# Performance work log

Measured on AMD Instinct MI355X. Metric: run time of the kernel, lower is better.

The kernel has to match this reference:

```python
import jax, jax.numpy as jnp
import numpy as np

N_HEADS = 16


def setup_inputs() -> dict:
    key = jax.random.key(0)
    bs, width, length = 2, 3072, 2048  # width = 3 * n_heads * ch, ch = 64
    qkv = jax.random.normal(key, (bs, width, length), dtype=jnp.float32)
    return {"qkv": qkv}


def reference(qkv):
    bs, width, length = qkv.shape
    ch = width // (3 * N_HEADS)
    # per-head layout within width is [q(ch), k(ch), v(ch)]
    qkv_h = qkv.reshape(bs * N_HEADS, 3 * ch, length)
    q, k, v = jnp.split(qkv_h, 3, axis=1)  # each [bs*H, ch, L]
    scale = 1.0 / jnp.sqrt(jnp.sqrt(jnp.asarray(ch, dtype=qkv.dtype)))
    # scores: [bs*H, L_q, L_k]
    weight = jnp.einsum('bct,bcs->bts', q * scale, k * scale)
    weight = jax.nn.softmax(weight.astype(jnp.float32), axis=-1).astype(qkv.dtype)
    a = jnp.einsum('bts,bcs->bct', weight, v)  # [bs*H, ch, L]
    return a.reshape(bs, -1, length)
```

## Files before the change

### kernel.cpp

```cpp
#include <hip/hip_runtime.h>
#include <hip/hip_bf16.h>
#include <stdint.h>

typedef float f32x4 __attribute__((ext_vector_type(4)));
typedef float f32x16 __attribute__((ext_vector_type(16)));
typedef __bf16 bf16x8 __attribute__((ext_vector_type(8)));
typedef uint32_t u32;
typedef u32 u32x4 __attribute__((ext_vector_type(4)));

#define SCALE 0.35355339059327378f
#define SCALE2 0.42466090014400953f
#define LOG2E 1.4426950408889634f

#if __has_builtin(__builtin_amdgcn_exp2f)
__device__ __forceinline__ float exp2fast(float x) { return __builtin_amdgcn_exp2f(x); }
#else
__device__ __forceinline__ float exp2fast(float x) { return exp2f(x); }
#endif

__device__ __forceinline__ u32 packbf2(float a, float b) {
  u32 ua = __builtin_bit_cast(u32, a);
  u32 ub = __builtin_bit_cast(u32, b);
  ua = (ua + 0x7fffu + ((ua >> 16) & 1u)) >> 16;
  ub = (ub + 0x7fffu + ((ub >> 16) & 1u)) >> 16;
  return ua | (ub << 16);
}
__device__ __forceinline__ unsigned short tobf(float a) {
  u32 ua = __builtin_bit_cast(u32, a);
  return (unsigned short)((ua + 0x7fffu + ((ua >> 16) & 1u)) >> 16);
}
__device__ __forceinline__ u32 pk2(float a, float b) {
  unsigned short lo = __builtin_bit_cast(unsigned short, (__bf16)a);
  unsigned short hi = __builtin_bit_cast(unsigned short, (__bf16)b);
  return (u32)lo | ((u32)hi << 16);
}
__device__ __forceinline__ int swz(int row, int col) {
  return row * 64 + (col ^ ((row & 7) << 3));
}
__device__ __forceinline__ void gload16(const void* g, void* l) {
  __builtin_amdgcn_global_load_lds((const __attribute__((address_space(1))) void*)g,
                                   (__attribute__((address_space(3))) void*)l, 16, 0, 0);
}
__device__ __forceinline__ f32x16 zero16() {
  f32x16 z;
#pragma unroll
  for (int i = 0; i < 16; ++i) z[i] = 0.f;
  return z;
}

__global__ __launch_bounds__(256) void prep_kernel(const float* __restrict__ qkv,
                                                   unsigned short* __restrict__ ws) {
  __shared__ unsigned short tq[64 * 64];
  __shared__ unsigned short tk[64 * 64];
  const int tid = threadIdx.x;
  const int bid = blockIdx.x;
  const int bh = bid >> 5;
  const int tile = bid & 31;
  const int b = bh >> 4, h = bh & 15;
  const float* hq = qkv + ((size_t)b * 3072 + (size_t)h * 192) * 2048;
  const int s0 = tile * 64;

  {
    const int c = tid >> 2;
    const int jj = (tid & 3) * 16;
    const float* qp = hq + (size_t)c * 2048 + s0 + jj;
    const float* kp = qp + 64 * 2048;
    const float* vp = qp + 128 * 2048;
    unsigned short* vout = ws + (size_t)64 * 131072 + (size_t)bh * 131072 +
                           (size_t)c * 2048 + s0 + jj;
    u32 vbuf[8];
#pragma unroll
    for (int u = 0; u < 4; ++u) {
      f32x4 fq = *(const f32x4*)(qp + u * 4);
      f32x4 fk = *(const f32x4*)(kp + u * 4);
      f32x4 fv = *(const f32x4*)(vp + u * 4);
#pragma unroll
      for (int e = 0; e < 4; ++e) {
        int s = jj + u * 4 + e;
        int sw = swz(s, c);
        tq[sw] = tobf(fq[e] * SCALE2);
        tk[sw] = tobf(fk[e] * SCALE2);
      }
      vbuf[2 * u]     = packbf2(fv[0], fv[1]);
      vbuf[2 * u + 1] = packbf2(fv[2], fv[3]);
    }
    *(u32x4*)(vout)     = *(u32x4*)&vbuf[0];
    *(u32x4*)(vout + 8) = *(u32x4*)&vbuf[4];
  }
  __syncthreads();
  {
    const int s = tid >> 2;
    const int c0 = (tid & 3) * 16;
    const int ch0 = (((c0 >> 3) ^ (s & 7)) << 3);
    const int ch1 = ((((c0 >> 3) + 1) ^ (s & 7)) << 3);
    size_t ob = (size_t)bh * 131072 + (size_t)(s0 + s) * 64 + c0;
    unsigned short* qout = ws + ob;
    unsigned short* kout = ws + (size_t)32 * 131072 + ob;
    *(u32x4*)qout       = *(u32x4*)&tq[s * 64 + ch0];
    *(u32x4*)(qout + 8) = *(u32x4*)&tq[s * 64 + ch1];
    *(u32x4*)kout       = *(u32x4*)&tk[s * 64 + ch0];
    *(u32x4*)(kout + 8) = *(u32x4*)&tk[s * 64 + ch1];
  }
}

__global__ __launch_bounds__(512, 4) void attn15_kernel(const unsigned short* __restrict__ ws,
                                                        float* __restrict__ out) {
  __shared__ __align__(16) char smem[66560];

  const int tid  = threadIdx.x;
  const int lane = tid & 63;
  const int wv   = tid >> 6;
  const int w4   = wv & 3;
  const int grp  = wv >> 2;
  const int l31  = lane & 31;
  const int hi   = lane >> 5;
  const int xr   = l31 & 7;
  const int xr2  = (l31 >> 3) & 3;

  const int bid = blockIdx.x;
  const int bh  = (bid & 7) * 4 + ((bid >> 3) >> 4);
  const int qb  = (bid >> 3) & 15;
  const int b = bh >> 4, h = bh & 15;

  const unsigned short* Qs = ws + (size_t)bh * 131072;
  const unsigned short* Ks = ws + (size_t)32 * 131072 + (size_t)bh * 131072;
  const unsigned short* Vs = ws + (size_t)64 * 131072 + (size_t)bh * 131072;

  bf16x8 qB[4];
#pragma unroll
  for (int kc = 0; kc < 4; ++kc)
    qB[kc] = *(const bf16x8*)(Qs + (size_t)(qb * 128 + w4 * 32 + l31) * 64 + kc * 16 + hi * 8);

  const int srow = lane >> 3;
  const int xa   = (2 * w4) & 3;
  const int sch0 = (lane & 7) ^ srow ^ xa;
  const int sch1 = sch0 ^ 1;
  const char* kgA = (const char*)Ks + (size_t)(w4 * 16 + srow) * 128      + sch0 * 16;
  const char* kgB = (const char*)Ks + (size_t)(w4 * 16 + 8 + srow) * 128  + sch1 * 16;
  const char* vgA = (const char*)Vs + (size_t)(w4 * 16 + srow) * 4096     + sch0 * 16;
  const char* vgB = (const char*)Vs + (size_t)(w4 * 16 + 8 + srow) * 4096 + sch1 * 16;
  char* kbase = smem + grp * 16384;
  char* vbase = smem + 32768 + grp * 16384;
  char* kd = kbase + w4 * 2048;
  char* vd = vbase + w4 * 2048;

  f32x16 oacc0 = zero16(), oacc1 = zero16();
  float lrun = 0.f;

  {
    gload16(kgA + (size_t)grp * 8192, kd);
    gload16(kgB + (size_t)grp * 8192, kd + 1024);
    gload16(vgA + (size_t)grp * 128,  vd);
    gload16(vgB + (size_t)grp * 128,  vd + 1024);
  }

#pragma unroll 1
  for (int it = 0; it < 16; ++it) {
    const int cur = it & 1;
    __syncthreads();
    if (it < 15) {
      const int stn = 2 * (it + 1) + grp;
      char* kdn = kd + (cur ^ 1) * 8192;
      char* vdn = vd + (cur ^ 1) * 8192;
      gload16(kgA + (size_t)stn * 8192, kdn);
      gload16(kgB + (size_t)stn * 8192, kdn + 1024);
      gload16(vgA + (size_t)stn * 128,  vdn);
      gload16(vgB + (size_t)stn * 128,  vdn + 1024);
    }

    const unsigned short* kt = (const unsigned short*)(kbase + cur * 8192);
    f32x16 a0 = zero16(), a1 = zero16();
    __builtin_amdgcn_s_setprio(1);
#pragma unroll
    for (int kc = 0; kc < 4; ++kc) {
      int chs = (((kc * 2 + hi) ^ xr ^ xr2)) << 3;
      bf16x8 kA0 = *(const bf16x8*)(kt + l31 * 64 + chs);
      bf16x8 kA1 = *(const bf16x8*)(kt + (32 + l31) * 64 + chs);
      a0 = __builtin_amdgcn_mfma_f32_32x32x16_bf16(kA0, qB[kc], a0, 0, 0, 0);
      a1 = __builtin_amdgcn_mfma_f32_32x32x16_bf16(kA1, qB[kc], a1, 0, 0, 0);
    }
    __builtin_amdgcn_s_setprio(0);

#pragma unroll
    for (int i = 0; i < 16; ++i) a0[i] = exp2fast(a0[i]);
#pragma unroll
    for (int i = 0; i < 16; ++i) a1[i] = exp2fast(a1[i]);
    {
      f32x16 s01 = a0 + a1;
      f32x4 s4;
#pragma unroll
      for (int i = 0; i < 4; ++i)
        s4[i] = (s01[i] + s01[i + 4]) + (s01[i + 8] + s01[i + 12]);
      lrun += (s4[0] + s4[1]) + (s4[2] + s4[3]);
    }

    bf16x8 pB[4];
#pragma unroll
    for (int sc = 0; sc < 4; ++sc) {
      const f32x16& src = (sc < 2) ? a0 : a1;
      const int rb = (sc & 1) * 8;
      u32 c01 = pk2(src[rb + 0], src[rb + 1]);
      u32 c23 = pk2(src[rb + 2], src[rb + 3]);
      u32 c45 = pk2(src[rb + 4], src[rb + 5]);
      u32 c67 = pk2(src[rb + 6], src[rb + 7]);
      asm volatile("v_permlane32_swap_b32 %0, %1" : "+v"(c01), "+v"(c45));
      asm volatile("v_permlane32_swap_b32 %0, %1" : "+v"(c23), "+v"(c67));
      u32x4 w = {c01, c23, c45, c67};
      pB[sc] = __builtin_bit_cast(bf16x8, w);
    }

    const unsigned short* vt = (const unsigned short*)(vbase + cur * 8192);
    __builtin_amdgcn_s_setprio(1);
#pragma unroll
    for (int sc = 0; sc < 4; ++sc) {
      int chs = (((sc * 2 + hi) ^ xr ^ xr2)) << 3;
      bf16x8 vA0 = *(const bf16x8*)(vt + l31 * 64 + chs);
      bf16x8 vA1 = *(const bf16x8*)(vt + (32 + l31) * 64 + chs);
      oacc0 = __builtin_amdgcn_mfma_f32_32x32x16_bf16(vA0, pB[sc], oacc0, 0, 0, 0);
      oacc1 = __builtin_amdgcn_mfma_f32_32x32x16_bf16(vA1, pB[sc], oacc1, 0, 0, 0);
    }
    __builtin_amdgcn_s_setprio(0);
  }

  float lfull = lrun + __shfl_xor(lrun, 32);
  __syncthreads();
  float* s_O = (float*)smem;
  float* s_l = (float*)(smem + 65536);
  if (grp == 1) {
    float* O1 = s_O + w4 * 2048;
#pragma unroll
    for (int r = 0; r < 16; ++r) {
      int c = (r & 3) + 8 * (r >> 2) + 4 * hi;
      O1[c * 32 + l31]        = oacc0[r];
      O1[(c + 32) * 32 + l31] = oacc1[r];
    }
    if (hi == 0) s_l[w4 * 32 + l31] = lfull;
  }
  __syncthreads();
  if (grp == 0) {
    float inv = 1.0f / (lfull + s_l[w4 * 32 + l31]);
    const float* O1 = s_O + w4 * 2048;
    float* outp = out + ((size_t)b * 1024 + (size_t)h * 64) * 2048;
    const int t = qb * 128 + w4 * 32 + l31;
#pragma unroll
    for (int r = 0; r < 16; ++r) {
      int c = (r & 3) + 8 * (r >> 2) + 4 * hi;
      outp[(size_t)c * 2048 + t]        = (oacc0[r] + O1[c * 32 + l31]) * inv;
      outp[(size_t)(c + 32) * 2048 + t] = (oacc1[r] + O1[(c + 32) * 32 + l31]) * inv;
    }
  }
}

__global__ __launch_bounds__(256) void qkv_attn_kernel(const float* __restrict__ qkv,
                                                       float* __restrict__ out) {
  __shared__ __align__(16) unsigned short s_kt[64 * 64];
  __shared__ __align__(16) unsigned short s_v [64 * 64];
  __shared__ __align__(16) unsigned short s_qp[128 * 64];

  const int tid  = threadIdx.x;
  const int lane = tid & 63;
  const int wv   = tid >> 6;
  const int l15  = lane & 15;
  const int lg   = lane >> 4;

  int bid = blockIdx.x;
  int bh  = (bid & 7) * 4 + ((bid >> 3) >> 4);
  int qb  = (bid >> 3) & 15;
  int b = bh >> 4, h = bh & 15;
  const float* __restrict__ hq = qkv + ((size_t)b * 3072 + (size_t)h * 192) * 2048;
  const int q0 = qb * 128;

  {
    int c  = (tid & 31) * 2;
    int tq = tid >> 5;
    const float* r0 = hq + (size_t)c * 2048 + q0;
    const float* r1 = r0 + 2048;
#pragma unroll
    for (int j = 0; j < 4; ++j) {
      int t4 = tq * 16 + j * 4;
      f32x4 f0 = *(const f32x4*)(r0 + t4);
      f32x4 f1 = *(const f32x4*)(r1 + t4);
#pragma unroll
      for (int e = 0; e < 4; ++e) {
        int t = t4 + e;
        ((u32*)s_qp)[swz(t, c) >> 1] = packbf2(f0[e] * SCALE, f1[e] * SCALE);
      }
    }
  }
  __syncthreads();

  bf16x8 qA[2][2];
#pragma unroll
  for (int tf = 0; tf < 2; ++tf)
#pragma unroll
    for (int kc = 0; kc < 2; ++kc) {
      int t  = wv * 32 + tf * 16 + l15;
      int c0 = kc * 32 + lg * 8;
      qA[tf][kc] = *(const bf16x8*)&s_qp[swz(t, c0)];
    }

  const f32x4 zf = {0.f, 0.f, 0.f, 0.f};
  f32x4 oacc[2][4];
#pragma unroll
  for (int tf = 0; tf < 2; ++tf)
#pragma unroll
    for (int cs = 0; cs < 4; ++cs) oacc[tf][cs] = zf;
  float mrun[2][4], lrun[2][4];
#pragma unroll
  for (int tf = 0; tf < 2; ++tf)
#pragma unroll
    for (int r = 0; r < 4; ++r) { mrun[tf][r] = -1e30f; lrun[tf][r] = 0.f; }

  const int pw = wv * 2048;

  for (int st = 0; st < 32; ++st) {
    const int s0g = st * 64;
    __syncthreads();
    {
      int c  = (tid & 31) * 2;
      int tq = tid >> 5;
      const float* r0 = hq + (size_t)(64 + c) * 2048 + s0g;
      const float* r1 = r0 + 2048;
#pragma unroll
      for (int j = 0; j < 2; ++j) {
        int s4 = tq * 8 + j * 4;
        f32x4 f0 = *(const f32x4*)(r0 + s4);
        f32x4 f1 = *(const f32x4*)(r1 + s4);
#pragma unroll
        for (int e = 0; e < 4; ++e)
          ((u32*)s_kt)[swz(s4 + e, c) >> 1] = packbf2(f0[e] * SCALE, f1[e] * SCALE);
      }
    }
    {
      int c  = tid >> 2;
      int sq = tid & 3;
      const float* rv = hq + (size_t)(128 + c) * 2048 + s0g;
#pragma unroll
      for (int j = 0; j < 4; ++j) {
        int s4 = sq * 16 + j * 4;
        f32x4 f = *(const f32x4*)(rv + s4);
        int si = swz(c, s4) >> 1;
        ((u32*)s_v)[si]     = packbf2(f[0], f[1]);
        ((u32*)s_v)[si + 1] = packbf2(f[2], f[3]);
      }
    }
    __syncthreads();

    f32x4 acc[2][4];
#pragma unroll
    for (int tf = 0; tf < 2; ++tf)
#pragma unroll
      for (int ss = 0; ss < 4; ++ss) acc[tf][ss] = zf;
#pragma unroll
    for (int kc = 0; kc < 2; ++kc) {
#pragma unroll
      for (int ss = 0; ss < 4; ++ss) {
        int srow = ss * 16 + l15;
        int c0   = kc * 32 + lg * 8;
        bf16x8 kB = *(const bf16x8*)&s_kt[swz(srow, c0)];
#pragma unroll
        for (int tf = 0; tf < 2; ++tf)
          acc[tf][ss] = __builtin_amdgcn_mfma_f32_16x16x32_bf16(qA[tf][kc], kB, acc[tf][ss], 0, 0, 0);
      }
    }

#pragma unroll
    for (int tf = 0; tf < 2; ++tf) {
#pragma unroll
      for (int r = 0; r < 4; ++r) {
        float tm = fmaxf(fmaxf(acc[tf][0][r], acc[tf][1][r]),
                         fmaxf(acc[tf][2][r], acc[tf][3][r]));
#pragma unroll
        for (int off = 1; off < 16; off <<= 1) tm = fmaxf(tm, __shfl_xor(tm, off));
        float mold = mrun[tf][r];
        float mnew = fmaxf(mold, tm);
        float rs   = exp2f((mold - mnew) * LOG2E);
        mrun[tf][r] = mnew;
        int t = tf * 16 + lg * 4 + r;
        float psum = 0.f;
#pragma unroll
        for (int ss = 0; ss < 4; ++ss) {
          float p = exp2f((acc[tf][ss][r] - mnew) * LOG2E);
          psum += p;
          s_qp[pw + swz(t, ss * 16 + l15)] = tobf(p);
        }
        lrun[tf][r] = lrun[tf][r] * rs + psum;
#pragma unroll
        for (int cs = 0; cs < 4; ++cs) oacc[tf][cs][r] *= rs;
      }
    }

    bf16x8 pA[2][2];
#pragma unroll
    for (int tf = 0; tf < 2; ++tf)
#pragma unroll
      for (int kc = 0; kc < 2; ++kc) {
        int t  = tf * 16 + l15;
        int s0 = kc * 32 + lg * 8;
        pA[tf][kc] = *(const bf16x8*)&s_qp[pw + swz(t, s0)];
      }
#pragma unroll
    for (int cs = 0; cs < 4; ++cs) {
#pragma unroll
      for (int kc = 0; kc < 2; ++kc) {
        int crow = cs * 16 + l15;
        int s0   = kc * 32 + lg * 8;
        bf16x8 vB = *(const bf16x8*)&s_v[swz(crow, s0)];
#pragma unroll
        for (int tf = 0; tf < 2; ++tf)
          oacc[tf][cs] = __builtin_amdgcn_mfma_f32_16x16x32_bf16(pA[tf][kc], vB, oacc[tf][cs], 0, 0, 0);
      }
    }
  }

  float* outp = out + ((size_t)b * 1024 + (size_t)h * 64) * 2048;
#pragma unroll
  for (int tf = 0; tf < 2; ++tf) {
    f32x4 invv;
#pragma unroll
    for (int r = 0; r < 4; ++r) {
      float ls = lrun[tf][r];
#pragma unroll
      for (int off = 1; off < 16; off <<= 1) ls += __shfl_xor(ls, off);
      invv[r] = 1.0f / ls;
    }
#pragma unroll
    for (int cs = 0; cs < 4; ++cs) {
      int c = cs * 16 + l15;
      float* po = outp + (size_t)c * 2048 + q0 + wv * 32 + tf * 16 + lg * 4;
      f32x4 o = oacc[tf][cs] * invv;
      *(f32x4*)po = o;
    }
  }
}

extern "C" void kernel_launch(void* const* d_in, const int* in_sizes, int n_in,
                              void* d_out, int out_size, void* d_ws, size_t ws_size,
                              hipStream_t stream) {
  (void)in_sizes; (void)n_in; (void)out_size;
  const float* qkv = (const float*)d_in[0];
  float* outp = (float*)d_out;
  const size_t need = (size_t)96 * 131072 * 2;
  if (ws_size >= need && d_ws != nullptr) {
    unsigned short* ws = (unsigned short*)d_ws;
    prep_kernel<<<dim3(1024), dim3(256), 0, stream>>>(qkv, ws);
    attn15_kernel<<<dim3(512), dim3(512), 0, stream>>>(ws, outp);
  } else {
    qkv_attn_kernel<<<dim3(512), dim3(256), 0, stream>>>(qkv, outp);
  }
}
```

Before: 63.89 us.

## Replace split-KV wave groups with 256-query blocks sharing full KV stream

Old kernel used 8 waves per block as two groups of four, each group processing half the key range for 128 queries, then merging partial outputs through shared memory. The new kernel gives each of 8 waves its own 32 queries (256 per block) and has all waves iterate over all 32 key tiles, sharing each K/V tile load across 8 waves. This removes the cross-group reduction and halves shared memory, doubling K/V reuse per load, but halves grid size to 256 blocks, which may underfill the GPU, and doubles the serial loop length per wave.

```diff
diff --git a/kernel.cpp b/kernel.cpp
--- a/kernel.cpp
+++ b/kernel.cpp
@@ -103,24 +103,23 @@
   }
 }
 
-__global__ __launch_bounds__(512, 4) void attn15_kernel(const unsigned short* __restrict__ ws,
+__global__ __launch_bounds__(512, 8) void attn16_kernel(const unsigned short* __restrict__ ws,
                                                         float* __restrict__ out) {
-  __shared__ __align__(16) char smem[66560];
+  __shared__ __align__(16) char smem[32768];
 
   const int tid  = threadIdx.x;
   const int lane = tid & 63;
   const int wv   = tid >> 6;
-  const int w4   = wv & 3;
-  const int grp  = wv >> 2;
   const int l31  = lane & 31;
   const int hi   = lane >> 5;
   const int xr   = l31 & 7;
   const int xr2  = (l31 >> 3) & 3;
 
   const int bid = blockIdx.x;
-  const int bh  = (bid & 7) * 4 + ((bid >> 3) >> 4);
-  const int qb  = (bid >> 3) & 15;
+  const int bh  = (bid & 7) * 4 + ((bid >> 3) >> 3);
+  const int qb  = (bid >> 3) & 7;
   const int b = bh >> 4, h = bh & 15;
+  const int q0 = qb * 256;
 
   const unsigned short* Qs = ws + (size_t)bh * 131072;
   const unsigned short* Ks = ws + (size_t)32 * 131072 + (size_t)bh * 131072;
@@ -129,46 +128,33 @@
   bf16x8 qB[4];
 #pragma unroll
   for (int kc = 0; kc < 4; ++kc)
-    qB[kc] = *(const bf16x8*)(Qs + (size_t)(qb * 128 + w4 * 32 + l31) * 64 + kc * 16 + hi * 8);
+    qB[kc] = *(const bf16x8*)(Qs + (size_t)(q0 + wv * 32 + l31) * 64 + kc * 16 + hi * 8);
 
   const int srow = lane >> 3;
-  const int xa   = (2 * w4) & 3;
-  const int sch0 = (lane & 7) ^ srow ^ xa;
-  const int sch1 = sch0 ^ 1;
-  const char* kgA = (const char*)Ks + (size_t)(w4 * 16 + srow) * 128      + sch0 * 16;
-  const char* kgB = (const char*)Ks + (size_t)(w4 * 16 + 8 + srow) * 128  + sch1 * 16;
-  const char* vgA = (const char*)Vs + (size_t)(w4 * 16 + srow) * 4096     + sch0 * 16;
-  const char* vgB = (const char*)Vs + (size_t)(w4 * 16 + 8 + srow) * 4096 + sch1 * 16;
-  char* kbase = smem + grp * 16384;
-  char* vbase = smem + 32768 + grp * 16384;
-  char* kd = kbase + w4 * 2048;
-  char* vd = vbase + w4 * 2048;
+  const int sch  = (lane & 7) ^ srow ^ (wv & 3);
+  const char* kg = (const char*)Ks + (size_t)(wv * 8 + srow) * 128  + sch * 16;
+  const char* vg = (const char*)Vs + (size_t)(wv * 8 + srow) * 4096 + sch * 16;
+  char* kd = smem + wv * 1024;
+  char* vd = smem + 16384 + wv * 1024;
 
   f32x16 oacc0 = zero16(), oacc1 = zero16();
   float lrun = 0.f;
 
   {
-    gload16(kgA + (size_t)grp * 8192, kd);
-    gload16(kgB + (size_t)grp * 8192, kd + 1024);
-    gload16(vgA + (size_t)grp * 128,  vd);
-    gload16(vgB + (size_t)grp * 128,  vd + 1024);
+    gload16(kg, kd);
+    gload16(vg, vd);
   }
 
 #pragma unroll 1
-  for (int it = 0; it < 16; ++it) {
+  for (int it = 0; it < 32; ++it) {
     const int cur = it & 1;
     __syncthreads();
-    if (it < 15) {
-      const int stn = 2 * (it + 1) + grp;
-      char* kdn = kd + (cur ^ 1) * 8192;
-      char* vdn = vd + (cur ^ 1) * 8192;
-      gload16(kgA + (size_t)stn * 8192, kdn);
-      gload16(kgB + (size_t)stn * 8192, kdn + 1024);
-      gload16(vgA + (size_t)stn * 128,  vdn);
-      gload16(vgB + (size_t)stn * 128,  vdn + 1024);
-    }
-
-    const unsigned short* kt = (const unsigned short*)(kbase + cur * 8192);
+    if (it < 31) {
+      gload16(kg + (size_t)(it + 1) * 8192, kd + (cur ^ 1) * 8192);
+      gload16(vg + (size_t)(it + 1) * 128,  vd + (cur ^ 1) * 8192);
+    }
+
+    const unsigned short* kt = (const unsigned short*)(smem + cur * 8192);
     f32x16 a0 = zero16(), a1 = zero16();
     __builtin_amdgcn_s_setprio(1);
 #pragma unroll
@@ -209,7 +195,7 @@
       pB[sc] = __builtin_bit_cast(bf16x8, w);
     }
 
-    const unsigned short* vt = (const unsigned short*)(vbase + cur * 8192);
+    const unsigned short* vt = (const unsigned short*)(smem + 16384 + cur * 8192);
     __builtin_amdgcn_s_setprio(1);
 #pragma unroll
     for (int sc = 0; sc < 4; ++sc) {
@@ -223,31 +209,14 @@
   }
 
   float lfull = lrun + __shfl_xor(lrun, 32);
-  __syncthreads();
-  float* s_O = (float*)smem;
-  float* s_l = (float*)(smem + 65536);
-  if (grp == 1) {
-    float* O1 = s_O + w4 * 2048;
-#pragma unroll
-    for (int r = 0; r < 16; ++r) {
-      int c = (r & 3) + 8 * (r >> 2) + 4 * hi;
-      O1[c * 32 + l31]        = oacc0[r];
-      O1[(c + 32) * 32 + l31] = oacc1[r];
-    }
-    if (hi == 0) s_l[w4 * 32 + l31] = lfull;
-  }
-  __syncthreads();
-  if (grp == 0) {
-    float inv = 1.0f / (lfull + s_l[w4 * 32 + l31]);
-    const float* O1 = s_O + w4 * 2048;
-    float* outp = out + ((size_t)b * 1024 + (size_t)h * 64) * 2048;
-    const int t = qb * 128 + w4 * 32 + l31;
-#pragma unroll
-    for (int r = 0; r < 16; ++r) {
-      int c = (r & 3) + 8 * (r >> 2) + 4 * hi;
-      outp[(size_t)c * 2048 + t]        = (oacc0[r] + O1[c * 32 + l31]) * inv;
-      outp[(size_t)(c + 32) * 2048 + t] = (oacc1[r] + O1[(c + 32) * 32 + l31]) * inv;
-    }
+  float inv = 1.0f / lfull;
+  float* outp = out + ((size_t)b * 1024 + (size_t)h * 64) * 2048;
+  const int t = q0 + wv * 32 + l31;
+#pragma unroll
+  for (int r = 0; r < 16; ++r) {
+    int c = (r & 3) + 8 * (r >> 2) + 4 * hi;
+    outp[(size_t)c * 2048 + t]        = oacc0[r] * inv;
+    outp[(size_t)(c + 32) * 2048 + t] = oacc1[r] * inv;
   }
 }
 
@@ -444,7 +413,7 @@
   if (ws_size >= need && d_ws != nullptr) {
     unsigned short* ws = (unsigned short*)d_ws;
     prep_kernel<<<dim3(1024), dim3(256), 0, stream>>>(qkv, ws);
-    attn15_kernel<<<dim3(512), dim3(512), 0, stream>>>(ws, outp);
+    attn16_kernel<<<dim3(256), dim3(512), 0, stream>>>(ws, outp);
   } else {
     qkv_attn_kernel<<<dim3(512), dim3(256), 0, stream>>>(qkv, outp);
   }
```

New measurement: 226.4 us. 3.54x slower.
